# Kernel tuning notes

Measured on AMD Instinct MI355X. Metric: run time of the kernel, lower is better.

Reference implementation:

```python
import jax, jax.numpy as jnp
import numpy as np

COST_CLASS = 1.0
COST_BBOX = 1.0
COST_GIOU = 1.0


def box_cxcywh_to_xyxy(b):
    cx, cy, w, h = jnp.split(b, 4, axis=-1)
    return jnp.concatenate([cx - 0.5 * w, cy - 0.5 * h, cx + 0.5 * w, cy + 0.5 * h], axis=-1)


def generalized_box_iou(b1, b2):
    # b1: [N,4] xyxy, b2: [M,4] xyxy -> [N,M]
    a1 = (b1[:, 2] - b1[:, 0]) * (b1[:, 3] - b1[:, 1])  # [N]
    a2 = (b2[:, 2] - b2[:, 0]) * (b2[:, 3] - b2[:, 1])  # [M]
    lt = jnp.maximum(b1[:, None, :2], b2[None, :, :2])  # [N,M,2]
    rb = jnp.minimum(b1[:, None, 2:], b2[None, :, 2:])
    wh = jnp.clip(rb - lt, 0.0)
    inter = wh[..., 0] * wh[..., 1]
    union = a1[:, None] + a2[None, :] - inter
    iou = inter / union
    lt_e = jnp.minimum(b1[:, None, :2], b2[None, :, :2])
    rb_e = jnp.maximum(b1[:, None, 2:], b2[None, :, 2:])
    wh_e = jnp.clip(rb_e - lt_e, 0.0)
    area = wh_e[..., 0] * wh_e[..., 1]
    return iou - (area - union) / area


def setup_inputs() -> dict:
    key = jax.random.key(0)
    k1, k2, k3, k4, k5 = jax.random.split(key, 5)
    bs, nq, d, total_tgt = 16, 900, 256, 1600
    return {
        "pred_logits": jax.random.normal(k1, (bs, nq, d), dtype=jnp.float32),
        "pred_boxes": jax.random.uniform(k2, (bs, nq, 4), dtype=jnp.float32),
        "tgt_embs": jax.random.normal(k3, (total_tgt, d), dtype=jnp.float32),
        "tgt_bbox": jax.random.uniform(k4, (total_tgt, 4), dtype=jnp.float32),
        "tgt_sizes": jax.random.randint(k5, (bs,), 0, 100, dtype=jnp.int32),  # only used by host-side LSA
    }


def reference(pred_logits, pred_boxes, tgt_embs, tgt_bbox, tgt_sizes):
    # Returns the sigmoid-squashed cost volume C [bs, num_queries, total_tgt];
    # scipy linear_sum_assignment over tgt_sizes splits is a host-side step.
    bs, nq = pred_logits.shape[:2]
    out_prob = pred_logits.reshape(bs * nq, -1)
    out_bbox = pred_boxes.reshape(bs * nq, 4)
    out_prob = out_prob / jnp.linalg.norm(out_prob, axis=-1, keepdims=True)
    cost_class = jax.nn.relu(out_prob @ tgt_embs.T)                    # [N,M]
    cost_bbox = jnp.sum(jnp.abs(out_bbox[:, None, :] - tgt_bbox[None, :, :]), axis=-1)  # L1 cdist
    cost_giou = -generalized_box_iou(box_cxcywh_to_xyxy(out_bbox), box_cxcywh_to_xyxy(tgt_bbox))
    C = COST_BBOX * cost_bbox + COST_CLASS * cost_class + COST_GIOU * cost_giou
    return jax.nn.sigmoid(C.reshape(bs, nq, -1))
```

## Files before the change

kernel.cpp:

```cpp
#include <hip/hip_runtime.h>

#define N_ROWS 14400
#define M_COLS 1600
#define KDIM   256
#define GRID_X 13
#define GRID_Y 113
#define NWG    (GRID_X * GRID_Y)

typedef __attribute__((ext_vector_type(8))) short bf16x8;
typedef __attribute__((ext_vector_type(4))) float f32x4;

__device__ __forceinline__ short f2bf(float x) {
  union { float f; unsigned u; } v; v.f = x;
  unsigned r = v.u + 0x7FFFu + ((v.u >> 16) & 1u);
  return (short)(r >> 16);
}

__device__ __forceinline__ void gload_lds16(const void* g, void* l) {
  __builtin_amdgcn_global_load_lds(
      (const __attribute__((address_space(1))) void*)g,
      (__attribute__((address_space(3))) void*)l, 16, 0, 0);
}

__global__ __launch_bounds__(256) void prep_kernel(
    const float* __restrict__ logits, const float* __restrict__ embs,
    short* __restrict__ probB, short* __restrict__ embB) {
  const int row = blockIdx.x * 4 + (threadIdx.x >> 6);
  const int lane = threadIdx.x & 63;
  if (row < N_ROWS) {
    const float4 x = ((const float4*)(logits + (size_t)row * KDIM))[lane];
    float s = x.x * x.x + x.y * x.y + x.z * x.z + x.w * x.w;
#pragma unroll
    for (int o = 32; o > 0; o >>= 1) s += __shfl_xor(s, o, 64);
    const float scale = __builtin_amdgcn_rsqf(s);
    short4 o4;
    o4.x = f2bf(x.x * scale); o4.y = f2bf(x.y * scale);
    o4.z = f2bf(x.z * scale); o4.w = f2bf(x.w * scale);
    ((short4*)(probB + (size_t)row * KDIM))[lane] = o4;
  } else {
    const int r = row - N_ROWS;
    const float4 x = ((const float4*)(embs + (size_t)r * KDIM))[lane];
    short4 o4;
    o4.x = f2bf(x.x); o4.y = f2bf(x.y); o4.z = f2bf(x.z); o4.w = f2bf(x.w);
    ((short4*)(embB + (size_t)r * KDIM))[lane] = o4;
  }
}

__global__ __launch_bounds__(256) void cost_kernel(
    const short* __restrict__ probB, const short* __restrict__ embB,
    const float* __restrict__ pbox, const float* __restrict__ tbox,
    float* __restrict__ out) {
  __shared__ short As[128 * 64];
  __shared__ short Bs[128 * 64];
  __shared__ f32x4 rowcc[128], rowxy[128], colcc[128], colxy[128];

  const int t = threadIdx.x;
  const int lane = t & 63;
  const int wid = t >> 6;
  const int wr = wid >> 1;
  const int wc = wid & 1;

  const int orig = blockIdx.x;
  const int xcd = orig & 7;
  const int rem = orig >> 3;
  const int q = NWG >> 3, r = NWG & 7;
  const int wgid = (xcd < r ? xcd * (q + 1) : r * (q + 1) + (xcd - r) * q) + rem;
  const int bx = wgid % GRID_X;
  const int by = wgid / GRID_X;
  const int rowBase = by * 128;
  const int colBase = bx * 128;

  {
    const bool isRow = (t < 128);
    const int idx = isRow ? (rowBase + t) : (colBase + t - 128);
    const int lim = isRow ? N_ROWS : M_COLS;
    const int cidx = idx < lim ? idx : lim - 1;
    const float4 bb = isRow ? ((const float4*)pbox)[cidx]
                            : ((const float4*)tbox)[cidx];
    f32x4 cc = {bb.x, bb.y, bb.z, bb.w};
    f32x4 xy = {fmaf(-0.5f, bb.z, bb.x), fmaf(-0.5f, bb.w, bb.y),
                fmaf(0.5f, bb.z, bb.x), fmaf(0.5f, bb.w, bb.y)};
    if (isRow) { rowcc[t] = cc; rowxy[t] = xy; }
    else       { colcc[t - 128] = cc; colxy[t - 128] = xy; }
  }

  f32x4 acc[4][4];
#pragma unroll
  for (int i = 0; i < 4; ++i)
#pragma unroll
    for (int j = 0; j < 4; ++j) acc[i][j] = (f32x4){0.f, 0.f, 0.f, 0.f};

  const int swz_gran = (lane & 7) ^ (lane >> 3);

  for (int kt = 0; kt < 4; ++kt) {
    const int k0 = kt * 64 + swz_gran * 8;
#pragma unroll
    for (int i = 0; i < 4; ++i) {
      const int rr = wid * 32 + i * 8 + (lane >> 3);
      int gr = rowBase + rr; if (gr > N_ROWS - 1) gr = N_ROWS - 1;
      gload_lds16(probB + (size_t)gr * KDIM + k0, As + (wid * 32 + i * 8) * 64);
      int gc = colBase + rr; if (gc > M_COLS - 1) gc = M_COLS - 1;
      gload_lds16(embB + (size_t)gc * KDIM + k0, Bs + (wid * 32 + i * 8) * 64);
    }
    __syncthreads();
#pragma unroll
    for (int kk = 0; kk < 2; ++kk) {
      bf16x8 af[4], bfr[4];
      const int g = kk * 4 + (lane >> 4);
#pragma unroll
      for (int mi = 0; mi < 4; ++mi) {
        const int row = wr * 64 + mi * 16 + (lane & 15);
        af[mi] = *(const bf16x8*)(As + row * 64 + ((g ^ (row & 7)) * 8));
      }
#pragma unroll
      for (int ni = 0; ni < 4; ++ni) {
        const int row = wc * 64 + ni * 16 + (lane & 15);
        bfr[ni] = *(const bf16x8*)(Bs + row * 64 + ((g ^ (row & 7)) * 8));
      }
#pragma unroll
      for (int mi = 0; mi < 4; ++mi)
#pragma unroll
        for (int ni = 0; ni < 4; ++ni)
          acc[mi][ni] = __builtin_amdgcn_mfma_f32_16x16x32_bf16(
              af[mi], bfr[ni], acc[mi][ni], 0, 0, 0);
    }
    __syncthreads();
  }

  const float LOG2E = 1.44269504f;
  const int colD = colBase + wc * 64 + (lane & 15);
#pragma unroll
  for (int mi = 0; mi < 4; ++mi) {
    f32x4 r0[4], r1[4];
    float ra[4];
    float* outp[4];
    bool rok[4];
#pragma unroll
    for (int j = 0; j < 4; ++j) {
      const int rloc = wr * 64 + mi * 16 + (lane >> 4) * 4 + j;
      const int gn = rowBase + rloc;
      rok[j] = (gn < N_ROWS);
      outp[j] = out + (size_t)gn * M_COLS + colD;
      r0[j] = rowcc[rloc];
      r1[j] = rowxy[rloc];
      ra[j] = r0[j][2] * r0[j][3];
    }
#pragma unroll
    for (int ni = 0; ni < 4; ++ni) {
      const int mloc = wc * 64 + ni * 16 + (lane & 15);
      const f32x4 c0 = colcc[mloc];
      const f32x4 c1 = colxy[mloc];
      const float ca = c0[2] * c0[3];
      const bool mok = (colBase + mloc < M_COLS);
#pragma unroll
      for (int j = 0; j < 4; ++j) {
        const float cc = fmaxf(acc[mi][ni][j], 0.0f);
        const float l1 = fabsf(r0[j][0] - c0[0]) + fabsf(r0[j][1] - c0[1]) +
                         fabsf(r0[j][2] - c0[2]) + fabsf(r0[j][3] - c0[3]);
        const float ltx = fmaxf(r1[j][0], c1[0]);
        const float lty = fmaxf(r1[j][1], c1[1]);
        const float rbx = fminf(r1[j][2], c1[2]);
        const float rby = fminf(r1[j][3], c1[3]);
        const float iw = fmaxf(rbx - ltx, 0.f);
        const float ih = fmaxf(rby - lty, 0.f);
        const float inter = iw * ih;
        const float uni = ra[j] + ca - inter;
        const float ex = fmaxf(r1[j][2], c1[2]) - fminf(r1[j][0], c1[0]);
        const float ey = fmaxf(r1[j][3], c1[3]) - fminf(r1[j][1], c1[1]);
        const float earea = ex * ey;
        const float Cv = l1 + cc + 1.0f
                         - inter * __builtin_amdgcn_rcpf(uni)
                         - uni * __builtin_amdgcn_rcpf(earea);
        const float sg = __builtin_amdgcn_rcpf(
            1.0f + __builtin_amdgcn_exp2f(-LOG2E * Cv));
        if (mok && rok[j])
          __builtin_nontemporal_store(sg, &outp[j][ni * 16]);
      }
    }
  }
}

extern "C" void kernel_launch(void* const* d_in, const int* in_sizes, int n_in,
                              void* d_out, int out_size, void* d_ws, size_t ws_size,
                              hipStream_t stream) {
  const float* logits = (const float*)d_in[0];
  const float* pbox   = (const float*)d_in[1];
  const float* embs   = (const float*)d_in[2];
  const float* tbox   = (const float*)d_in[3];
  float* out = (float*)d_out;

  short* probB = (short*)d_ws;
  short* embB  = probB + (size_t)N_ROWS * KDIM;

  prep_kernel<<<(N_ROWS + M_COLS) / 4, 256, 0, stream>>>(logits, embs, probB, embB);

  cost_kernel<<<NWG, 256, 0, stream>>>(probB, embB, pbox, tbox, out);
}
```

Baseline: 52.81 us.

## Shrink column tile to 64 and stage epilogue through LDS for vector stores

Tiles change from 128x128 to 128x64, which removes the wasted padded column tile (1600 = 25*64) and roughly doubles the workgroup count. The epilogue now writes sigmoid results into LDS, reusing the A tile buffer, and then emits coalesced 16-byte nontemporal row stores instead of scattered scalar stores. This costs extra syncthreads per row block and more reads of the A operand.

```diff
diff --git a/kernel.cpp b/kernel.cpp
--- a/kernel.cpp
+++ b/kernel.cpp
@@ -3,7 +3,7 @@
 #define N_ROWS 14400
 #define M_COLS 1600
 #define KDIM   256
-#define GRID_X 13
+#define GRID_X 25
 #define GRID_Y 113
 #define NWG    (GRID_X * GRID_Y)
 
@@ -51,8 +51,10 @@
     const float* __restrict__ pbox, const float* __restrict__ tbox,
     float* __restrict__ out) {
   __shared__ short As[128 * 64];
-  __shared__ short Bs[128 * 64];
-  __shared__ f32x4 rowcc[128], rowxy[128], colcc[128], colxy[128];
+  __shared__ short Bs[64 * 64];
+  __shared__ f32x4 rowcc[128], rowxy[128];
+  __shared__ f32x4 colcc[64],  colxy[64];
+  float* const tbuf = (float*)As;
 
   const int t = threadIdx.x;
   const int lane = t & 63;
@@ -68,44 +70,49 @@
   const int bx = wgid % GRID_X;
   const int by = wgid / GRID_X;
   const int rowBase = by * 128;
-  const int colBase = bx * 128;
-
-  {
-    const bool isRow = (t < 128);
-    const int idx = isRow ? (rowBase + t) : (colBase + t - 128);
-    const int lim = isRow ? N_ROWS : M_COLS;
-    const int cidx = idx < lim ? idx : lim - 1;
-    const float4 bb = isRow ? ((const float4*)pbox)[cidx]
-                            : ((const float4*)tbox)[cidx];
-    f32x4 cc = {bb.x, bb.y, bb.z, bb.w};
-    f32x4 xy = {fmaf(-0.5f, bb.z, bb.x), fmaf(-0.5f, bb.w, bb.y),
-                fmaf(0.5f, bb.z, bb.x), fmaf(0.5f, bb.w, bb.y)};
-    if (isRow) { rowcc[t] = cc; rowxy[t] = xy; }
-    else       { colcc[t - 128] = cc; colxy[t - 128] = xy; }
-  }
-
-  f32x4 acc[4][4];
+  const int colBase = bx * 64;
+
+  if (t < 128) {
+    const int idx = rowBase + t;
+    const int ci = idx < N_ROWS ? idx : N_ROWS - 1;
+    const float4 bb = ((const float4*)pbox)[ci];
+    rowcc[t] = (f32x4){bb.x, bb.y, bb.z, bb.w};
+    rowxy[t] = (f32x4){fmaf(-0.5f, bb.z, bb.x), fmaf(-0.5f, bb.w, bb.y),
+                       fmaf(0.5f, bb.z, bb.x), fmaf(0.5f, bb.w, bb.y)};
+  } else if (t < 192) {
+    const int c = t - 128;
+    const float4 bb = ((const float4*)tbox)[colBase + c];
+    colcc[c] = (f32x4){bb.x, bb.y, bb.z, bb.w};
+    colxy[c] = (f32x4){fmaf(-0.5f, bb.z, bb.x), fmaf(-0.5f, bb.w, bb.y),
+                       fmaf(0.5f, bb.z, bb.x), fmaf(0.5f, bb.w, bb.y)};
+  }
+
+  f32x4 acc[4][2];
 #pragma unroll
   for (int i = 0; i < 4; ++i)
 #pragma unroll
-    for (int j = 0; j < 4; ++j) acc[i][j] = (f32x4){0.f, 0.f, 0.f, 0.f};
-
-  const int swz_gran = (lane & 7) ^ (lane >> 3);
+    for (int j = 0; j < 2; ++j) acc[i][j] = (f32x4){0.f, 0.f, 0.f, 0.f};
+
+  const int swz = (lane & 7) ^ (lane >> 3);
+  const int rbase = wid * 8 + (lane >> 3);
 
   for (int kt = 0; kt < 4; ++kt) {
-    const int k0 = kt * 64 + swz_gran * 8;
+    const int k0 = kt * 64 + swz * 8;
 #pragma unroll
     for (int i = 0; i < 4; ++i) {
-      const int rr = wid * 32 + i * 8 + (lane >> 3);
-      int gr = rowBase + rr; if (gr > N_ROWS - 1) gr = N_ROWS - 1;
-      gload_lds16(probB + (size_t)gr * KDIM + k0, As + (wid * 32 + i * 8) * 64);
-      int gc = colBase + rr; if (gc > M_COLS - 1) gc = M_COLS - 1;
-      gload_lds16(embB + (size_t)gc * KDIM + k0, Bs + (wid * 32 + i * 8) * 64);
+      int gr = rowBase + i * 32 + rbase;
+      if (gr > N_ROWS - 1) gr = N_ROWS - 1;
+      gload_lds16(probB + (size_t)gr * KDIM + k0, As + (i * 32 + wid * 8) * 64);
+    }
+#pragma unroll
+    for (int i = 0; i < 2; ++i) {
+      const int gc = colBase + i * 32 + rbase;
+      gload_lds16(embB + (size_t)gc * KDIM + k0, Bs + (i * 32 + wid * 8) * 64);
     }
     __syncthreads();
 #pragma unroll
     for (int kk = 0; kk < 2; ++kk) {
-      bf16x8 af[4], bfr[4];
+      bf16x8 af[4], bfr[2];
       const int g = kk * 4 + (lane >> 4);
 #pragma unroll
       for (int mi = 0; mi < 4; ++mi) {
@@ -113,14 +120,14 @@
         af[mi] = *(const bf16x8*)(As + row * 64 + ((g ^ (row & 7)) * 8));
       }
 #pragma unroll
-      for (int ni = 0; ni < 4; ++ni) {
-        const int row = wc * 64 + ni * 16 + (lane & 15);
+      for (int ni = 0; ni < 2; ++ni) {
+        const int row = wc * 32 + ni * 16 + (lane & 15);
         bfr[ni] = *(const bf16x8*)(Bs + row * 64 + ((g ^ (row & 7)) * 8));
       }
 #pragma unroll
       for (int mi = 0; mi < 4; ++mi)
 #pragma unroll
-        for (int ni = 0; ni < 4; ++ni)
+        for (int ni = 0; ni < 2; ++ni)
           acc[mi][ni] = __builtin_amdgcn_mfma_f32_16x16x32_bf16(
               af[mi], bfr[ni], acc[mi][ni], 0, 0, 0);
     }
@@ -128,55 +135,64 @@
   }
 
   const float LOG2E = 1.44269504f;
-  const int colD = colBase + wc * 64 + (lane & 15);
+  const int jr = (lane >> 4) * 4;
+  const int lc = lane & 15;
+  f32x4 c0v[2], c1v[2];
+  float cav[2];
+#pragma unroll
+  for (int ni = 0; ni < 2; ++ni) {
+    const int cloc = wc * 32 + ni * 16 + lc;
+    c0v[ni] = colcc[cloc];
+    c1v[ni] = colxy[cloc];
+    cav[ni] = c0v[ni][2] * c0v[ni][3];
+  }
+
 #pragma unroll
   for (int mi = 0; mi < 4; ++mi) {
-    f32x4 r0[4], r1[4];
-    float ra[4];
-    float* outp[4];
-    bool rok[4];
 #pragma unroll
     for (int j = 0; j < 4; ++j) {
-      const int rloc = wr * 64 + mi * 16 + (lane >> 4) * 4 + j;
-      const int gn = rowBase + rloc;
-      rok[j] = (gn < N_ROWS);
-      outp[j] = out + (size_t)gn * M_COLS + colD;
-      r0[j] = rowcc[rloc];
-      r1[j] = rowxy[rloc];
-      ra[j] = r0[j][2] * r0[j][3];
-    }
-#pragma unroll
-    for (int ni = 0; ni < 4; ++ni) {
-      const int mloc = wc * 64 + ni * 16 + (lane & 15);
-      const f32x4 c0 = colcc[mloc];
-      const f32x4 c1 = colxy[mloc];
-      const float ca = c0[2] * c0[3];
-      const bool mok = (colBase + mloc < M_COLS);
-#pragma unroll
-      for (int j = 0; j < 4; ++j) {
+      const int rloc = wr * 64 + mi * 16 + jr + j;
+      const f32x4 r0 = rowcc[rloc];
+      const f32x4 r1 = rowxy[rloc];
+      const float ra = r0[2] * r0[3];
+#pragma unroll
+      for (int ni = 0; ni < 2; ++ni) {
+        const f32x4 c0 = c0v[ni], c1 = c1v[ni];
         const float cc = fmaxf(acc[mi][ni][j], 0.0f);
-        const float l1 = fabsf(r0[j][0] - c0[0]) + fabsf(r0[j][1] - c0[1]) +
-                         fabsf(r0[j][2] - c0[2]) + fabsf(r0[j][3] - c0[3]);
-        const float ltx = fmaxf(r1[j][0], c1[0]);
-        const float lty = fmaxf(r1[j][1], c1[1]);
-        const float rbx = fminf(r1[j][2], c1[2]);
-        const float rby = fminf(r1[j][3], c1[3]);
+        const float l1 = fabsf(r0[0] - c0[0]) + fabsf(r0[1] - c0[1]) +
+                         fabsf(r0[2] - c0[2]) + fabsf(r0[3] - c0[3]);
+        const float ltx = fmaxf(r1[0], c1[0]);
+        const float lty = fmaxf(r1[1], c1[1]);
+        const float rbx = fminf(r1[2], c1[2]);
+        const float rby = fminf(r1[3], c1[3]);
         const float iw = fmaxf(rbx - ltx, 0.f);
         const float ih = fmaxf(rby - lty, 0.f);
         const float inter = iw * ih;
-        const float uni = ra[j] + ca - inter;
-        const float ex = fmaxf(r1[j][2], c1[2]) - fminf(r1[j][0], c1[0]);
-        const float ey = fmaxf(r1[j][3], c1[3]) - fminf(r1[j][1], c1[1]);
+        const float uni = ra + cav[ni] - inter;
+        const float ex = fmaxf(r1[2], c1[2]) - fminf(r1[0], c1[0]);
+        const float ey = fmaxf(r1[3], c1[3]) - fminf(r1[1], c1[1]);
         const float earea = ex * ey;
         const float Cv = l1 + cc + 1.0f
                          - inter * __builtin_amdgcn_rcpf(uni)
                          - uni * __builtin_amdgcn_rcpf(earea);
         const float sg = __builtin_amdgcn_rcpf(
             1.0f + __builtin_amdgcn_exp2f(-LOG2E * Cv));
-        if (mok && rok[j])
-          __builtin_nontemporal_store(sg, &outp[j][ni * 16]);
+        tbuf[(wr * 16 + jr + j) * 68 + wc * 32 + ni * 16 + lc] = sg;
       }
     }
+    __syncthreads();
+#pragma unroll
+    for (int rr = 0; rr < 2; ++rr) {
+      const int rch = rr * 16 + (t >> 4);
+      const int c4 = (t & 15) * 4;
+      const f32x4 v = *(const f32x4*)(tbuf + rch * 68 + c4);
+      const int grow = rowBase + ((rch < 16) ? (mi * 16 + rch)
+                                             : (64 + mi * 16 + (rch - 16)));
+      if (grow < N_ROWS)
+        __builtin_nontemporal_store(
+            v, (f32x4*)(out + (size_t)grow * M_COLS + colBase + c4));
+    }
+    __syncthreads();
   }
 }
 
```

New measurement: 49.26 us. -6.7%, faster.
